# Optimization experiments

Measured on AMD Instinct MI355X. Metric: run time of the kernel, lower is better.

Reference implementation:

```python
import jax, jax.numpy as jnp
import numpy as np

L = 16            # n_levels
F = 2             # n_features_per_level
T = 2 ** 20       # hashmap size (power of 2)
N_MIN = 16.0
SCALE = 1.26
PI1 = np.uint32(1)
PI2 = np.uint32(2654435761)
N_PTS = 2097152


def setup_inputs() -> dict:
    key = jax.random.key(0)
    k1, k2 = jax.random.split(key)
    x = jax.random.uniform(k1, (N_PTS, 2), dtype=jnp.float32)
    # torch.rand(T,F,L)*2e-4 - 1e-4
    hash_table = jax.random.uniform(k2, (T, F, L), dtype=jnp.float32) * 0.0002 - 0.0001
    return {"x": x, "hash_table": hash_table}


def _hash(ix, iy):
    # torch does int64 xor then % T; since T=2^20 divides 2^32 and coords are
    # nonnegative, uint32 wraparound arithmetic gives identical low bits.
    return (jnp.bitwise_xor(ix * PI1, iy * PI2) % jnp.uint32(T)).astype(jnp.int32)


def _encode(x, hash_table):
    n = x.shape[0]
    # per-level resolutions, floor(N_min * b^l), computed in fp32 like torch
    NL = jnp.floor(N_MIN * jnp.power(jnp.float32(SCALE), jnp.arange(L, dtype=jnp.float32)))  # [L]
    xNL = x[:, :, None] * NL                      # [N, 2, L]
    xi = xNL.astype(jnp.int32)                    # trunc == floor for x >= 0
    local = xNL - xi.astype(xNL.dtype)            # [N, 2, L]
    ix = xi[:, 0, :].astype(jnp.uint32)           # [N, L]
    iy = xi[:, 1, :].astype(jnp.uint32)
    h0 = _hash(ix, iy)
    h1 = _hash(ix + 1, iy)
    h2 = _hash(ix, iy + 1)
    h3 = _hash(ix + 1, iy + 1)
    # hash_table[T,F,L] -> [L,T,F] so we can gather per (level, hash) pair
    Ht = jnp.transpose(hash_table, (2, 0, 1))     # [L, T, F]
    lev = jnp.broadcast_to(jnp.arange(L), h0.shape)  # [N, L]
    H0 = Ht[lev, h0]                              # [N, L, F]
    H1 = Ht[lev, h1]
    H2 = Ht[lev, h2]
    H3 = Ht[lev, h3]
    x1 = local[:, 0, :][:, :, None]               # [N, L, 1]
    x2 = local[:, 1, :][:, :, None]
    y = ((1 - x1) * (1 - x2) * H0 + x1 * (1 - x2) * H1
         + (1 - x1) * x2 * H2 + x1 * x2 * H3)     # [N, L, F]
    return y.reshape(n, L * F)


def reference(x, hash_table):
    return _encode(x, hash_table)
```

## Files before the change

kernel.cpp:

```cpp
#include <hip/hip_runtime.h>

#define NLEVELS 16
#define TMASK 0xFFFFFu
#define PI2 2654435761u
#define DENSE_TOTAL 711664u
#define DBLK 2780
#define NBUCK 4096
#define NPARTS 256

typedef float vfloat4 __attribute__((ext_vector_type(4)));

__constant__ float c_NL[NLEVELS] = {
    16.f, 20.f, 25.f, 32.f, 40.f, 50.f, 64.f, 80.f,
    101.f, 128.f, 161.f, 203.f, 256.f, 322.f, 406.f, 512.f
};

__device__ __forceinline__ unsigned bf16rn(float f) {
    unsigned u = __float_as_uint(f);
    return (u + 0x7FFFu + ((u >> 16) & 1u)) >> 16;
}

__global__ __launch_bounds__(256) void build_hist_kernel(
    const float* __restrict__ tb, unsigned* __restrict__ dense,
    const float2* __restrict__ x, int* __restrict__ h, int npts, int chunk)
{
    __shared__ int sh[NBUCK];
    if (blockIdx.x < DBLK) {
        constexpr unsigned kOFF[16] = {0u,289u,730u,1406u,2495u,4176u,6777u,11002u,
            17563u,27967u,44608u,70852u,112468u,178517u,282846u,448495u};
        constexpr unsigned kW[16] = {17u,21u,26u,33u,41u,51u,65u,81u,
            102u,129u,162u,204u,257u,323u,407u,513u};
        unsigned e = blockIdx.x * 256u + threadIdx.x;
        if (e >= DENSE_TOTAL) return;
        unsigned off = 0u, w = 17u; int l = 0;
        #pragma unroll
        for (int k = 1; k < 16; ++k)
            if (e >= kOFF[k]) { off = kOFF[k]; w = kW[k]; l = k; }
        unsigned rem = e - off;
        unsigned cy = rem / w;
        unsigned cx = rem - cy * w;
        unsigned hh = (cx ^ (cy * PI2)) & TMASK;
        float f0 = tb[(size_t)hh * 32 + l];
        float f1 = tb[(size_t)hh * 32 + 16 + l];
        dense[e] = bf16rn(f0) | (bf16rn(f1) << 16);
    } else {
        for (int i = threadIdx.x; i < NBUCK; i += 256) sh[i] = 0;
        __syncthreads();
        int b = blockIdx.x - DBLK;
        int start = b * chunk;
        int end = min(npts, start + chunk);
        for (int i = start + (int)threadIdx.x; i < end; i += 256) {
            float2 p = x[i];
            int bx = min(63, (int)(p.x * 64.f));
            int by = min(63, (int)(p.y * 64.f));
            atomicAdd(&sh[by * 64 + bx], 1);
        }
        __syncthreads();
        int* hb = h + (size_t)b * NBUCK;
        for (int i = threadIdx.x; i < NBUCK; i += 256) hb[i] = sh[i];
    }
}

__global__ __launch_bounds__(256) void binsum_kernel(
    const int* __restrict__ h, int* __restrict__ tot)
{
    int bin = blockIdx.x * 256 + threadIdx.x;
    int acc = 0;
    for (int b = 0; b < NPARTS; ++b) acc += h[(size_t)b * NBUCK + bin];
    tot[bin] = acc;
}

__global__ __launch_bounds__(1024) void scan_kernel(
    const int* __restrict__ tot, int* __restrict__ base)
{
    __shared__ int s[1024];
    int t = threadIdx.x;
    int v[4], pre[4], sum = 0;
    #pragma unroll
    for (int j = 0; j < 4; ++j) {
        v[j] = tot[t * 4 + j];
        pre[j] = sum;
        sum += v[j];
    }
    s[t] = sum;
    __syncthreads();
    for (int d = 1; d < 1024; d <<= 1) {
        int a = (t >= d) ? s[t - d] : 0;
        __syncthreads();
        s[t] += a;
        __syncthreads();
    }
    int bb = s[t] - sum;
    #pragma unroll
    for (int j = 0; j < 4; ++j)
        base[t * 4 + j] = bb + pre[j];
}

__global__ __launch_bounds__(256) void binoff_kernel(
    const int* __restrict__ h, const int* __restrict__ base,
    int* __restrict__ off)
{
    int bin = blockIdx.x * 256 + threadIdx.x;
    int acc = base[bin];
    for (int b = 0; b < NPARTS; ++b) {
        off[(size_t)b * NBUCK + bin] = acc;
        acc += h[(size_t)b * NBUCK + bin];
    }
}

__global__ __launch_bounds__(256) void scatter_part_kernel(
    const float2* __restrict__ x, const int* __restrict__ off,
    uint4* __restrict__ xsidx, int npts, int chunk)
{
    __shared__ int cnt[NBUCK];
    int b = blockIdx.x;
    const int* ob = off + (size_t)b * NBUCK;
    for (int i = threadIdx.x; i < NBUCK; i += 256) cnt[i] = ob[i];
    __syncthreads();
    int start = b * chunk;
    int end = min(npts, start + chunk);
    for (int i = start + (int)threadIdx.x; i < end; i += 256) {
        float2 p = x[i];
        int bx = min(63, (int)(p.x * 64.f));
        int by = min(63, (int)(p.y * 64.f));
        int pos = atomicAdd(&cnt[by * 64 + bx], 1);
        xsidx[pos] = make_uint4(__float_as_uint(p.x), __float_as_uint(p.y),
                                (unsigned)i, 0u);
    }
}

__global__ __launch_bounds__(256) void encode_sorted_dense_kernel(
    const uint4* __restrict__ xsidx, const unsigned* __restrict__ dense,
    vfloat4* __restrict__ out, int npts)
{
    constexpr unsigned kOFF[16] = {0u,289u,730u,1406u,2495u,4176u,6777u,11002u,
        17563u,27967u,44608u,70852u,112468u,178517u,282846u,448495u};
    constexpr int kW[16] = {17,21,26,33,41,51,65,81,102,129,162,204,257,323,407,513};

    __shared__ vfloat4 stg[256 * 9];
    __shared__ int soi[256];

    int i = blockIdx.x * 256 + threadIdx.x;
    vfloat4 res[8];
    int oi = -1;
    if (i < npts) {
        uint4 rec = xsidx[i];
        float2 p = make_float2(__uint_as_float(rec.x), __uint_as_float(rec.y));
        oi = (int)rec.z;
        #pragma unroll
        for (int g = 0; g < 2; ++g) {
            unsigned long long Hlo[8], Hhi[8];
            float lxv[8], lyv[8];
            #pragma unroll
            for (int k = 0; k < 8; ++k) {
                const int l = g * 8 + k;
                float nl = c_NL[l];
                float fx = p.x * nl;
                float fy = p.y * nl;
                int ix = (int)fx;
                int iy = (int)fy;
                lxv[k] = fx - (float)ix;
                lyv[k] = fy - (float)iy;
                const unsigned* grid = dense + kOFF[l];
                int b = iy * kW[l] + ix;
                __builtin_memcpy(&Hlo[k], grid + b, 8);
                __builtin_memcpy(&Hhi[k], grid + b + kW[l], 8);
            }
            #pragma unroll
            for (int k = 0; k < 8; k += 2) {
                float r[4];
                #pragma unroll
                for (int m = 0; m < 2; ++m) {
                    float lx = lxv[k + m], ly = lyv[k + m];
                    float w0 = (1.f - lx) * (1.f - ly);
                    float w1 = lx * (1.f - ly);
                    float w2 = (1.f - lx) * ly;
                    float w3 = lx * ly;
                    unsigned u0 = (unsigned)Hlo[k + m];
                    unsigned u1 = (unsigned)(Hlo[k + m] >> 32);
                    unsigned u2 = (unsigned)Hhi[k + m];
                    unsigned u3 = (unsigned)(Hhi[k + m] >> 32);
                    float a0 = __uint_as_float(u0 << 16), b0 = __uint_as_float(u0 & 0xFFFF0000u);
                    float a1 = __uint_as_float(u1 << 16), b1 = __uint_as_float(u1 & 0xFFFF0000u);
                    float a2 = __uint_as_float(u2 << 16), b2 = __uint_as_float(u2 & 0xFFFF0000u);
                    float a3 = __uint_as_float(u3 << 16), b3 = __uint_as_float(u3 & 0xFFFF0000u);
                    r[2*m]   = w0*a0 + w1*a1 + w2*a2 + w3*a3;
                    r[2*m+1] = w0*b0 + w1*b1 + w2*b2 + w3*b3;
                }
                vfloat4 v; v.x = r[0]; v.y = r[1]; v.z = r[2]; v.w = r[3];
                res[g * 4 + (k >> 1)] = v;
            }
        }
    } else {
        #pragma unroll
        for (int k = 0; k < 8; ++k) res[k] = (vfloat4)(0.f);
    }

    soi[threadIdx.x] = oi;
    #pragma unroll
    for (int k = 0; k < 8; ++k) stg[threadIdx.x * 9 + k] = res[k];
    __syncthreads();

    int r0 = threadIdx.x >> 3;
    int j  = threadIdx.x & 7;
    #pragma unroll
    for (int p = 0; p < 8; ++p) {
        int row = p * 32 + r0;
        int o = soi[row];
        if (o >= 0)
            __builtin_nontemporal_store(stg[row * 9 + j], out + (size_t)o * 8 + j);
    }
}

__global__ __launch_bounds__(256) void hashgrid_kernel(
    const float2* __restrict__ x, const float* __restrict__ tb,
    float2* __restrict__ out, int npts)
{
    int tid = blockIdx.x * blockDim.x + threadIdx.x;
    int n = tid >> 4;
    int l = tid & 15;
    if (n >= npts) return;

    float2 xy = x[n];
    float nl = c_NL[l];
    float fx = xy.x * nl;
    float fy = xy.y * nl;
    int ixi = (int)fx;
    int iyi = (int)fy;
    float lx = fx - (float)ixi;
    float ly = fy - (float)iyi;
    unsigned ix = (unsigned)ixi, iy = (unsigned)iyi;

    unsigned hy0 = iy * PI2;
    unsigned hy1 = (iy + 1u) * PI2;
    unsigned h0 = (ix        ^ hy0) & TMASK;
    unsigned h1 = ((ix + 1u) ^ hy0) & TMASK;
    unsigned h2 = (ix        ^ hy1) & TMASK;
    unsigned h3 = ((ix + 1u) ^ hy1) & TMASK;

    const float* p0 = tb + ((size_t)h0 * 32 + l);
    const float* p1 = tb + ((size_t)h1 * 32 + l);
    const float* p2 = tb + ((size_t)h2 * 32 + l);
    const float* p3 = tb + ((size_t)h3 * 32 + l);
    float a0 = p0[0], b0 = p0[16];
    float a1 = p1[0], b1 = p1[16];
    float a2 = p2[0], b2 = p2[16];
    float a3 = p3[0], b3 = p3[16];

    float w0 = (1.f - lx) * (1.f - ly);
    float w1 = lx * (1.f - ly);
    float w2 = (1.f - lx) * ly;
    float w3 = lx * ly;
    float o0 = w0 * a0 + w1 * a1 + w2 * a2 + w3 * a3;
    float o1 = w0 * b0 + w1 * b1 + w2 * b2 + w3 * b3;

    out[(size_t)n * NLEVELS + l] = make_float2(o0, o1);
}

extern "C" void kernel_launch(void* const* d_in, const int* in_sizes, int n_in,
                              void* d_out, int out_size, void* d_ws, size_t ws_size,
                              hipStream_t stream) {
    const float2* x = (const float2*)d_in[0];
    const float* tb = (const float*)d_in[1];
    int npts = in_sizes[0] / 2;

    size_t dense_bytes = ((size_t)DENSE_TOTAL * 4 + 255) & ~(size_t)255;
    size_t xsidx_off   = dense_bytes;
    size_t xsidx_bytes = ((size_t)npts * 16 + 255) & ~(size_t)255;
    size_t h_off       = xsidx_off + xsidx_bytes;
    size_t h_bytes     = (size_t)NPARTS * NBUCK * 4;
    size_t tot_off     = h_off + h_bytes;
    size_t tot_bytes   = NBUCK * 4;
    size_t base_off    = tot_off + tot_bytes;
    size_t off_off     = base_off + tot_bytes;
    size_t need        = off_off + h_bytes;

    if (ws_size >= need) {
        char* ws = (char*)d_ws;
        unsigned* dense = (unsigned*)ws;
        uint4* xsidx  = (uint4*)(ws + xsidx_off);
        int* h        = (int*)(ws + h_off);
        int* tot      = (int*)(ws + tot_off);
        int* base     = (int*)(ws + base_off);
        int* off      = (int*)(ws + off_off);

        int chunk = (npts + NPARTS - 1) / NPARTS;
        int nblk = (npts + 255) / 256;

        build_hist_kernel<<<DBLK + NPARTS, 256, 0, stream>>>(tb, dense, x, h, npts, chunk);
        binsum_kernel<<<NBUCK / 256, 256, 0, stream>>>(h, tot);
        scan_kernel<<<1, 1024, 0, stream>>>(tot, base);
        binoff_kernel<<<NBUCK / 256, 256, 0, stream>>>(h, base, off);
        scatter_part_kernel<<<NPARTS, 256, 0, stream>>>(x, off, xsidx, npts, chunk);
        encode_sorted_dense_kernel<<<nblk, 256, 0, stream>>>(
            xsidx, dense, (vfloat4*)d_out, npts);
    } else {
        long long total = (long long)npts * NLEVELS;
        long long grid = (total + 255) / 256;
        hashgrid_kernel<<<(int)grid, 256, 0, stream>>>(x, tb, (float2*)d_out, npts);
    }
}
```

Before: 134.7 us.

## Build dense level grids from one master grid and narrow histogram counts

The dense-table build now runs one thread per cell of a 513x513 master grid. Each thread reads the full 32-float hash-table row for its cell once and writes the bf16-packed entry for every level whose grid contains that cell, exploiting that all levels share the same hash of (cx,cy). Previously each level's cells did a separate scattered gather, two floats at a time. The per-partition histogram is also stored as 16-bit counts, halving the traffic of the binsum and binoff passes. The trade-off is a wider 128-byte load per thread and scattered multi-level writes, and the 16-bit counts rely on no partition bin exceeding 65535.

```diff
diff --git a/kernel.cpp b/kernel.cpp
--- a/kernel.cpp
+++ b/kernel.cpp
@@ -4,7 +4,9 @@
 #define TMASK 0xFFFFFu
 #define PI2 2654435761u
 #define DENSE_TOTAL 711664u
-#define DBLK 2780
+#define MASTER 513
+#define MASTER_TOTAL (513u * 513u)
+#define GBLK 1029
 #define NBUCK 4096
 #define NPARTS 256
 
@@ -22,31 +24,32 @@
 
 __global__ __launch_bounds__(256) void build_hist_kernel(
     const float* __restrict__ tb, unsigned* __restrict__ dense,
-    const float2* __restrict__ x, int* __restrict__ h, int npts, int chunk)
+    const float2* __restrict__ x, unsigned short* __restrict__ h,
+    int npts, int chunk)
 {
     __shared__ int sh[NBUCK];
-    if (blockIdx.x < DBLK) {
+    if (blockIdx.x < GBLK) {
         constexpr unsigned kOFF[16] = {0u,289u,730u,1406u,2495u,4176u,6777u,11002u,
             17563u,27967u,44608u,70852u,112468u,178517u,282846u,448495u};
         constexpr unsigned kW[16] = {17u,21u,26u,33u,41u,51u,65u,81u,
             102u,129u,162u,204u,257u,323u,407u,513u};
         unsigned e = blockIdx.x * 256u + threadIdx.x;
-        if (e >= DENSE_TOTAL) return;
-        unsigned off = 0u, w = 17u; int l = 0;
+        if (e >= MASTER_TOTAL) return;
+        unsigned cy = e / MASTER;
+        unsigned cx = e - cy * MASTER;
+        unsigned hh = (cx ^ (cy * PI2)) & TMASK;
+        float v[32];
+        __builtin_memcpy(v, tb + (size_t)hh * 32, 128);
         #pragma unroll
-        for (int k = 1; k < 16; ++k)
-            if (e >= kOFF[k]) { off = kOFF[k]; w = kW[k]; l = k; }
-        unsigned rem = e - off;
-        unsigned cy = rem / w;
-        unsigned cx = rem - cy * w;
-        unsigned hh = (cx ^ (cy * PI2)) & TMASK;
-        float f0 = tb[(size_t)hh * 32 + l];
-        float f1 = tb[(size_t)hh * 32 + 16 + l];
-        dense[e] = bf16rn(f0) | (bf16rn(f1) << 16);
+        for (int l = 0; l < 16; ++l) {
+            unsigned W = kW[l];
+            if (cx < W && cy < W)
+                dense[kOFF[l] + cy * W + cx] = bf16rn(v[l]) | (bf16rn(v[16 + l]) << 16);
+        }
     } else {
         for (int i = threadIdx.x; i < NBUCK; i += 256) sh[i] = 0;
         __syncthreads();
-        int b = blockIdx.x - DBLK;
+        int b = blockIdx.x - GBLK;
         int start = b * chunk;
         int end = min(npts, start + chunk);
         for (int i = start + (int)threadIdx.x; i < end; i += 256) {
@@ -56,13 +59,14 @@
             atomicAdd(&sh[by * 64 + bx], 1);
         }
         __syncthreads();
-        int* hb = h + (size_t)b * NBUCK;
-        for (int i = threadIdx.x; i < NBUCK; i += 256) hb[i] = sh[i];
+        unsigned short* hb = h + (size_t)b * NBUCK;
+        for (int i = threadIdx.x; i < NBUCK; i += 256)
+            hb[i] = (unsigned short)sh[i];
     }
 }
 
 __global__ __launch_bounds__(256) void binsum_kernel(
-    const int* __restrict__ h, int* __restrict__ tot)
+    const unsigned short* __restrict__ h, int* __restrict__ tot)
 {
     int bin = blockIdx.x * 256 + threadIdx.x;
     int acc = 0;
@@ -97,7 +101,7 @@
 }
 
 __global__ __launch_bounds__(256) void binoff_kernel(
-    const int* __restrict__ h, const int* __restrict__ base,
+    const unsigned short* __restrict__ h, const int* __restrict__ base,
     int* __restrict__ off)
 {
     int bin = blockIdx.x * 256 + threadIdx.x;
@@ -268,26 +272,26 @@
     size_t xsidx_off   = dense_bytes;
     size_t xsidx_bytes = ((size_t)npts * 16 + 255) & ~(size_t)255;
     size_t h_off       = xsidx_off + xsidx_bytes;
-    size_t h_bytes     = (size_t)NPARTS * NBUCK * 4;
+    size_t h_bytes     = ((size_t)NPARTS * NBUCK * 2 + 255) & ~(size_t)255;
     size_t tot_off     = h_off + h_bytes;
     size_t tot_bytes   = NBUCK * 4;
     size_t base_off    = tot_off + tot_bytes;
     size_t off_off     = base_off + tot_bytes;
-    size_t need        = off_off + h_bytes;
+    size_t need        = off_off + (size_t)NPARTS * NBUCK * 4;
 
     if (ws_size >= need) {
         char* ws = (char*)d_ws;
         unsigned* dense = (unsigned*)ws;
-        uint4* xsidx  = (uint4*)(ws + xsidx_off);
-        int* h        = (int*)(ws + h_off);
-        int* tot      = (int*)(ws + tot_off);
-        int* base     = (int*)(ws + base_off);
-        int* off      = (int*)(ws + off_off);
+        uint4* xsidx    = (uint4*)(ws + xsidx_off);
+        unsigned short* h = (unsigned short*)(ws + h_off);
+        int* tot        = (int*)(ws + tot_off);
+        int* base       = (int*)(ws + base_off);
+        int* off        = (int*)(ws + off_off);
 
         int chunk = (npts + NPARTS - 1) / NPARTS;
         int nblk = (npts + 255) / 256;
 
-        build_hist_kernel<<<DBLK + NPARTS, 256, 0, stream>>>(tb, dense, x, h, npts, chunk);
+        build_hist_kernel<<<GBLK + NPARTS, 256, 0, stream>>>(tb, dense, x, h, npts, chunk);
         binsum_kernel<<<NBUCK / 256, 256, 0, stream>>>(h, tot);
         scan_kernel<<<1, 1024, 0, stream>>>(tot, base);
         binoff_kernel<<<NBUCK / 256, 256, 0, stream>>>(h, base, off);
```

Measured after the change: 129.2 us (median of 2 runs). -4.1%, faster.
